# Kernel optimization log

Hardware: AMD Instinct MI355X
Metric: run time of the kernel (lower is better)

## Reference

```python
import jax, jax.numpy as jnp
import numpy as np

B, L, H2, P, A, T = 2048, 128, 600, 50, 50, 3  # batch, seq, 2*hidden, pos_emb, attn, latent types


def setup_inputs() -> dict:
    key = jax.random.key(0)
    ks = jax.random.split(key, 9)
    return {
        "hidden": jax.random.normal(ks[0], (B, L, H2), dtype=jnp.float32),
        "pos1_emb": jax.random.normal(ks[1], (B, L, P), dtype=jnp.float32),
        "pos2_emb": jax.random.normal(ks[2], (B, L, P), dtype=jnp.float32),
        "entity1_idx": jax.random.randint(ks[3], (B,), 0, L),
        "entity2_idx": jax.random.randint(ks[4], (B,), 0, L),
        "W_hid": jax.random.normal(ks[5], (A, H2 + 2 * P), dtype=jnp.float32) * 0.05,
        "W_ent": jax.random.normal(ks[6], (A, 4 * H2), dtype=jnp.float32) * 0.05,
        "latent_types": jax.random.normal(ks[7], (T, H2), dtype=jnp.float32) * 0.05,
        "v": jax.random.normal(ks[8], (A, 1), dtype=jnp.float32) * 0.05,
    }


def _latent_type(ent, latent_types):
    # ent: [B, 1, H2]; latent_types: [T, H2]
    a = jax.nn.softmax(jnp.einsum("bed,td->bet", ent, latent_types), axis=-1)
    return jnp.einsum("bet,td->bed", a, latent_types)  # [B, 1, H2]


def reference(hidden, pos1_emb, pos2_emb, entity1_idx, entity2_idx, W_hid, W_ent, latent_types, v):
    b = hidden.shape[0]
    batch_ix = jnp.arange(b)
    hid_e1 = hidden[batch_ix, entity1_idx][:, None, :]  # [B, 1, H2]
    hid_e2 = hidden[batch_ix, entity2_idx][:, None, :]
    e1_type = _latent_type(hid_e1, latent_types)
    e2_type = _latent_type(hid_e2, latent_types)
    # u1: per-token projection, u2: per-sentence entity projection (broadcast over L)
    u1 = jnp.einsum("bld,ad->bla", jnp.concatenate([hidden, pos1_emb, pos2_emb], axis=-1), W_hid)
    u2 = jnp.einsum("bed,ad->bea", jnp.concatenate([hid_e1, e1_type, hid_e2, e2_type], axis=-1), W_ent)
    u = jnp.tanh(u1 + u2)  # [B, L, A]
    scores = jnp.einsum("bla,a->bl", u, v[:, 0])  # [B, L]
    alpha = jax.nn.softmax(scores, axis=-1)
    z = jnp.einsum("bl,bld->bd", alpha, hidden)  # [B, H2]
    return z
```

## Files before the change

kernel.cpp:

```cpp
#include <hip/hip_runtime.h>
#include <hip/hip_bf16.h>
#include <math.h>


#define B_    2048
#define L_    128
#define H2_   600
#define P_    50
#define A_    50
#define D700  700
#define KCN   22
#define KH    11
#define AP    64
#define MT    16
#define XP    712

typedef __attribute__((ext_vector_type(8))) short short8;
typedef __attribute__((ext_vector_type(4))) float f32x4;

__device__ __forceinline__ unsigned short f2bf(float f) {
  unsigned u = __float_as_uint(f);
  u += 0x7fffu + ((u >> 16) & 1u);
  return (unsigned short)(u >> 16);
}
__device__ __forceinline__ unsigned pk2(float lo, float hi) {
  return (unsigned)f2bf(lo) | ((unsigned)f2bf(hi) << 16);
}
__device__ __forceinline__ float bf2f(unsigned short s) {
  return __uint_as_float(((unsigned)s) << 16);
}

__global__ __launch_bounds__(256) void kwprep(const float* __restrict__ Wh,
                                              unsigned short* __restrict__ Wt) {
  int idx = blockIdx.x * 256 + threadIdx.x;
  if (idx >= KCN * 2048) return;
  int kc = idx >> 11, r = idx & 2047, a = r >> 5, kk = r & 31;
  int d = kc * 32 + kk;
  float v = (a < A_ && d < D700) ? Wh[a * D700 + d] : 0.f;
  Wt[idx] = f2bf(v);
}

__global__ __launch_bounds__(256) void ku2(const float* __restrict__ hidden,
                                           const int* __restrict__ e1,
                                           const int* __restrict__ e2,
                                           const float* __restrict__ Went,
                                           const float* __restrict__ lt,
                                           float* __restrict__ u2ws) {
  __shared__ __align__(16) float E[2][2400];
  __shared__ float dots[2][2][3];
  __shared__ float aw[2][2][3];
  int tid = threadIdx.x;
  int b0 = blockIdx.x * 2;

  for (int idx = tid; idx < 2 * 2 * 150; idx += 256) {
    int i = idx / 300, r = idx - i * 300, e = r / 150, g = r - e * 150;
    int bb = b0 + i;
    int l = e ? e2[bb] : e1[bb];
    float4 f = *(const float4*)(hidden + ((size_t)bb * L_ + l) * H2_ + g * 4);
    *(float4*)(&E[i][e * 1200 + g * 4]) = f;
  }
  __syncthreads();

  int w = tid >> 6, lane = tid & 63;
  for (int task = w * 3; task < w * 3 + 3; ++task) {
    int i = task / 6, e = (task / 3) & 1, t = task % 3;
    float p = 0.f;
    for (int d = lane; d < 600; d += 64) p += E[i][e * 1200 + d] * lt[t * 600 + d];
    #pragma unroll
    for (int mask = 1; mask <= 32; mask <<= 1) p += __shfl_xor(p, mask);
    if (lane == 0) dots[i][e][t] = p;
  }
  __syncthreads();
  if (tid < 12) {
    int t = tid % 3, e = (tid / 3) & 1, i = tid / 6;
    float d0 = dots[i][e][0], d1 = dots[i][e][1], d2 = dots[i][e][2];
    float m = fmaxf(d0, fmaxf(d1, d2));
    float x0 = expf(d0 - m), x1 = expf(d1 - m), x2 = expf(d2 - m);
    float Z = x0 + x1 + x2;
    aw[i][e][t] = ((t == 0) ? x0 : (t == 1) ? x1 : x2) / Z;
  }
  __syncthreads();
  for (int idx = tid; idx < 2 * 2 * 600; idx += 256) {
    int i = idx / 1200, r = idx - i * 1200, e = r / 600, d = r - e * 600;
    float v = aw[i][e][0] * lt[d] + aw[i][e][1] * lt[600 + d] + aw[i][e][2] * lt[1200 + d];
    E[i][e * 1200 + 600 + d] = v;
  }
  __syncthreads();
  for (int a = w; a < A_; a += 4) {
    float acc[2] = {0.f, 0.f};
    for (int d0 = lane * 4; d0 < 2400; d0 += 256) {
      float4 wv = *(const float4*)(Went + a * 2400 + d0);
      #pragma unroll
      for (int i = 0; i < 2; ++i) {
        float4 ev = *(const float4*)(&E[i][d0]);
        acc[i] += ev.x * wv.x + ev.y * wv.y + ev.z * wv.z + ev.w * wv.w;
      }
    }
    #pragma unroll
    for (int i = 0; i < 2; ++i) {
      float p = acc[i];
      #pragma unroll
      for (int mask = 1; mask <= 32; mask <<= 1) p += __shfl_xor(p, mask);
      if (lane == 0) u2ws[(b0 + i) * AP + a] = p;
    }
  }
  for (int idx = tid; idx < 2 * (AP - A_); idx += 256) {
    u2ws[(b0 + idx / (AP - A_)) * AP + A_ + idx % (AP - A_)] = 0.f;
  }
}

__global__ __launch_bounds__(256, 4) void kmain(
    const float* __restrict__ hidden, const float* __restrict__ pos1,
    const float* __restrict__ pos2, const float* __restrict__ vvec,
    const unsigned short* __restrict__ Wt, const float* __restrict__ u2ws,
    float* __restrict__ zp_ws, float* __restrict__ mS_ws) {
  __shared__ __align__(16) unsigned short Xs[MT * XP];
  __shared__ float scores4[4][MT];
  __shared__ float es_s[MT];
  __shared__ float u2s[AP];
  __shared__ float vs[AP];

  int tid = threadIdx.x;
  int bq = blockIdx.x;
  int b = bq >> 3, o = bq & 7, tok0 = o * MT;
  int lane = tid & 63, wv = tid >> 6;
  int acol = lane & 15, kgrp = lane >> 4;

  int t = tid >> 4, c0 = tid & 15;
  const float* rowp = hidden + ((size_t)(b * L_ + tok0) + t) * H2_;
  float4 f[9];
  #pragma unroll
  for (int j = 0; j < 9; ++j) f[j] = *(const float4*)(rowp + (c0 + 16 * j) * 4);
  bool h10 = (c0 < 6);
  float4 f9;
  if (h10) f9 = *(const float4*)(rowp + (c0 + 144) * 4);

  const float* p1 = pos1 + (size_t)(b * L_ + tok0) * P_;
  const float* p2 = pos2 + (size_t)(b * L_ + tok0) * P_;
  float2 q1a = *(const float2*)(p1 + tid * 2);
  float2 q2a = *(const float2*)(p2 + tid * 2);
  bool hq = (tid < 144);
  float2 q1b, q2b;
  if (hq) {
    q1b = *(const float2*)(p1 + (tid + 256) * 2);
    q2b = *(const float2*)(p2 + (tid + 256) * 2);
  }
  float u2v = 0.f, vvv = 0.f;
  if (tid < AP) {
    u2v = u2ws[b * AP + tid];
    vvv = (tid < A_) ? vvec[tid] : 0.f;
  }
  const unsigned short* wbase = Wt + (wv * 16 + acol) * 32 + kgrp * 8;
  short8 wf1[KH];
  #pragma unroll
  for (int kc = 0; kc < KH; ++kc)
    wf1[kc] = *(const short8*)(wbase + kc * 2048);

  #pragma unroll
  for (int j = 0; j < 9; ++j) {
    uint2 w; w.x = pk2(f[j].x, f[j].y); w.y = pk2(f[j].z, f[j].w);
    *(uint2*)(&Xs[t * XP + (c0 + 16 * j) * 4]) = w;
  }
  if (h10) {
    uint2 w; w.x = pk2(f9.x, f9.y); w.y = pk2(f9.z, f9.w);
    *(uint2*)(&Xs[t * XP + (c0 + 144) * 4]) = w;
  }
  {
    int t1 = tid / 25, g = tid - t1 * 25;
    *(unsigned*)(&Xs[t1 * XP + 600 + g * 2]) = pk2(q1a.x, q1a.y);
    *(unsigned*)(&Xs[t1 * XP + 650 + g * 2]) = pk2(q2a.x, q2a.y);
  }
  if (hq) {
    int idx = tid + 256;
    int t1 = idx / 25, g = idx - t1 * 25;
    *(unsigned*)(&Xs[t1 * XP + 600 + g * 2]) = pk2(q1b.x, q1b.y);
    *(unsigned*)(&Xs[t1 * XP + 650 + g * 2]) = pk2(q2b.x, q2b.y);
  }
  if (tid < MT * 2) {
    int tt = tid >> 1, g = tid & 1;
    *(unsigned*)(&Xs[tt * XP + 700 + g * 2]) = 0u;
  }
  if (tid < AP) { u2s[tid] = u2v; vs[tid] = vvv; }
  __syncthreads();

  short8 wf2[KH];
  #pragma unroll
  for (int kc = 0; kc < KH; ++kc)
    wf2[kc] = *(const short8*)(wbase + (KH + kc) * 2048);

  f32x4 acc0 = {0.f, 0.f, 0.f, 0.f};
  #pragma unroll
  for (int kc = 0; kc < KH; ++kc) {
    short8 a0 = *(const short8*)(&Xs[acol * XP + kc * 32 + kgrp * 8]);
    acc0 = __builtin_amdgcn_mfma_f32_16x16x32_bf16(a0, wf1[kc], acc0, 0, 0, 0);
  }
  #pragma unroll
  for (int kc = 0; kc < KH; ++kc) {
    short8 a0 = *(const short8*)(&Xs[acol * XP + (KH + kc) * 32 + kgrp * 8]);
    acc0 = __builtin_amdgcn_mfma_f32_16x16x32_bf16(a0, wf2[kc], acc0, 0, 0, 0);
  }

  {
    float va = vs[wv * 16 + acol];
    float u2a = u2s[wv * 16 + acol];
    float s0[4];
    #pragma unroll
    for (int r = 0; r < 4; ++r) s0[r] = va * tanhf(acc0[r] + u2a);
    #pragma unroll
    for (int mask = 1; mask < 16; mask <<= 1) {
      #pragma unroll
      for (int r = 0; r < 4; ++r) s0[r] += __shfl_xor(s0[r], mask);
    }
    if (acol == 0) {
      #pragma unroll
      for (int r = 0; r < 4; ++r) scores4[wv][kgrp * 4 + r] = s0[r];
    }
  }
  __syncthreads();

  if (tid < 64) {
    float s = (tid < MT)
                  ? (scores4[0][tid] + scores4[1][tid] + scores4[2][tid] + scores4[3][tid])
                  : -3.402823466e38f;
    float m = s;
    #pragma unroll
    for (int mask = 1; mask <= 32; mask <<= 1) m = fmaxf(m, __shfl_xor(m, mask));
    float e = (tid < MT) ? expf(s - m) : 0.f;
    float S = e;
    #pragma unroll
    for (int mask = 1; mask <= 32; mask <<= 1) S += __shfl_xor(S, mask);
    if (tid < MT) es_s[tid] = e;
    if (tid == 0) { mS_ws[bq * 2] = m; mS_ws[bq * 2 + 1] = S; }
  }
  __syncthreads();

  if (tid < 75) {
    float acc[8] = {0.f, 0.f, 0.f, 0.f, 0.f, 0.f, 0.f, 0.f};
    #pragma unroll
    for (int tt = 0; tt < MT; ++tt) {
      short8 xv = *(const short8*)(&Xs[tt * XP + tid * 8]);
      float e = es_s[tt];
      #pragma unroll
      for (int j = 0; j < 8; ++j) acc[j] += e * bf2f((unsigned short)xv[j]);
    }
    float4 w0 = {acc[0], acc[1], acc[2], acc[3]};
    float4 w1 = {acc[4], acc[5], acc[6], acc[7]};
    *(float4*)(zp_ws + (size_t)bq * 600 + tid * 8) = w0;
    *(float4*)(zp_ws + (size_t)bq * 600 + tid * 8 + 4) = w1;
  }
}

__global__ __launch_bounds__(128) void kcomb(const float* __restrict__ zp_ws,
                                             const float* __restrict__ mS_ws,
                                             float* __restrict__ out) {
  int b = blockIdx.x, tid = threadIdx.x;
  float mq[8], Sq[8];
  #pragma unroll
  for (int qq = 0; qq < 8; ++qq) {
    mq[qq] = mS_ws[(b * 8 + qq) * 2];
    Sq[qq] = mS_ws[(b * 8 + qq) * 2 + 1];
  }
  float M = mq[0];
  #pragma unroll
  for (int qq = 1; qq < 8; ++qq) M = fmaxf(M, mq[qq]);
  float c[8], Z = 0.f;
  #pragma unroll
  for (int qq = 0; qq < 8; ++qq) { c[qq] = expf(mq[qq] - M); Z += Sq[qq] * c[qq]; }
  float inv = 1.f / Z;
  for (int d = tid; d < 600; d += 128) {
    float z = 0.f;
    #pragma unroll
    for (int qq = 0; qq < 8; ++qq) z += c[qq] * zp_ws[(size_t)(b * 8 + qq) * 600 + d];
    out[b * 600 + d] = z * inv;
  }
}

extern "C" void kernel_launch(void* const* d_in, const int* in_sizes, int n_in,
                              void* d_out, int out_size, void* d_ws, size_t ws_size,
                              hipStream_t stream) {
  const float* hidden = (const float*)d_in[0];
  const float* pos1   = (const float*)d_in[1];
  const float* pos2   = (const float*)d_in[2];
  const int*   e1     = (const int*)d_in[3];
  const int*   e2     = (const int*)d_in[4];
  const float* Whid   = (const float*)d_in[5];
  const float* Went   = (const float*)d_in[6];
  const float* lt     = (const float*)d_in[7];
  const float* vvec   = (const float*)d_in[8];
  float* out = (float*)d_out;

  char* ws = (char*)d_ws;
  unsigned short* Wt = (unsigned short*)ws;
  float* u2ws  = (float*)(ws + 98304);
  float* mS_ws = (float*)(ws + 98304 + 524288);
  float* zp_ws = (float*)(ws + 98304 + 524288 + 131072);

  hipLaunchKernelGGL(kwprep, dim3(176), dim3(256), 0, stream, Whid, Wt);
  hipLaunchKernelGGL(ku2, dim3(B_ / 2), dim3(256), 0, stream, hidden, e1, e2, Went, lt, u2ws);
  hipLaunchKernelGGL(kmain, dim3(B_ * 8), dim3(256), 0, stream, hidden, pos1, pos2, vvec,
                     Wt, u2ws, zp_ws, mS_ws);
  hipLaunchKernelGGL(kcomb, dim3(B_), dim3(128), 0, stream, zp_ws, mS_ws, out);
}
```

Measured before the change: 272.5 us.

## Make kmain persistent with double-buffered LDS prefetch of next tile

Converts kmain into a persistent kernel with a fixed grid of 768 blocks that loops over token tiles. Each block loads the W fragments into registers once, then prefetches the next tile's hidden and pos rows into a second LDS buffer while it computes the current tile's MFMA, tanh, softmax and weighted sum. The goal is to hide global memory latency and avoid reloading weights for every tile. The cost is twice the LDS, more registers (launch bounds lowered to 3 blocks per SM), and fewer resident blocks, which could reduce memory-level parallelism.

```diff
diff --git a/kernel.cpp b/kernel.cpp
--- a/kernel.cpp
+++ b/kernel.cpp
@@ -10,10 +10,11 @@
 #define A_    50
 #define D700  700
 #define KCN   22
-#define KH    11
 #define AP    64
 #define MT    16
 #define XP    712
+#define GRIDM 768
+#define NBQ   (B_ * 8)
 
 typedef __attribute__((ext_vector_type(8))) short short8;
 typedef __attribute__((ext_vector_type(4))) float f32x4;
@@ -109,144 +110,195 @@
   }
 }
 
-__global__ __launch_bounds__(256, 4) void kmain(
+__global__ __launch_bounds__(256, 3) void kmain(
     const float* __restrict__ hidden, const float* __restrict__ pos1,
     const float* __restrict__ pos2, const float* __restrict__ vvec,
     const unsigned short* __restrict__ Wt, const float* __restrict__ u2ws,
     float* __restrict__ zp_ws, float* __restrict__ mS_ws) {
-  __shared__ __align__(16) unsigned short Xs[MT * XP];
+  __shared__ __align__(16) unsigned short Xs[2][MT * XP];
   __shared__ float scores4[4][MT];
   __shared__ float es_s[MT];
-  __shared__ float u2s[AP];
-  __shared__ float vs[AP];
 
   int tid = threadIdx.x;
+  int lane = tid & 63, wvix = tid >> 6;
+  int acol = lane & 15, kgrp = lane >> 4;
+  int t = tid >> 4, c0 = tid & 15;
+  bool h10 = (c0 < 6);
+  bool hq = (tid < 144);
+  int aidx = wvix * 16 + acol;
+
+  const unsigned short* wbase = Wt + aidx * 32 + kgrp * 8;
+  short8 wf[KCN];
+  #pragma unroll
+  for (int kc = 0; kc < KCN; ++kc) wf[kc] = *(const short8*)(wbase + kc * 2048);
+  float va = (aidx < A_) ? vvec[aidx] : 0.f;
+
+  if (tid < 64) {
+    int hh = tid >> 5, r = tid & 31, rr = r >> 1, g = r & 1;
+    *(unsigned*)(&Xs[hh][rr * XP + 700 + g * 2]) = 0u;
+  }
+
   int bq = blockIdx.x;
-  int b = bq >> 3, o = bq & 7, tok0 = o * MT;
-  int lane = tid & 63, wv = tid >> 6;
-  int acol = lane & 15, kgrp = lane >> 4;
-
-  int t = tid >> 4, c0 = tid & 15;
-  const float* rowp = hidden + ((size_t)(b * L_ + tok0) + t) * H2_;
-  float4 f[9];
-  #pragma unroll
-  for (int j = 0; j < 9; ++j) f[j] = *(const float4*)(rowp + (c0 + 16 * j) * 4);
-  bool h10 = (c0 < 6);
-  float4 f9;
-  if (h10) f9 = *(const float4*)(rowp + (c0 + 144) * 4);
-
-  const float* p1 = pos1 + (size_t)(b * L_ + tok0) * P_;
-  const float* p2 = pos2 + (size_t)(b * L_ + tok0) * P_;
-  float2 q1a = *(const float2*)(p1 + tid * 2);
-  float2 q2a = *(const float2*)(p2 + tid * 2);
-  bool hq = (tid < 144);
-  float2 q1b, q2b;
-  if (hq) {
-    q1b = *(const float2*)(p1 + (tid + 256) * 2);
-    q2b = *(const float2*)(p2 + (tid + 256) * 2);
-  }
-  float u2v = 0.f, vvv = 0.f;
-  if (tid < AP) {
-    u2v = u2ws[b * AP + tid];
-    vvv = (tid < A_) ? vvec[tid] : 0.f;
-  }
-  const unsigned short* wbase = Wt + (wv * 16 + acol) * 32 + kgrp * 8;
-  short8 wf1[KH];
-  #pragma unroll
-  for (int kc = 0; kc < KH; ++kc)
-    wf1[kc] = *(const short8*)(wbase + kc * 2048);
-
-  #pragma unroll
-  for (int j = 0; j < 9; ++j) {
-    uint2 w; w.x = pk2(f[j].x, f[j].y); w.y = pk2(f[j].z, f[j].w);
-    *(uint2*)(&Xs[t * XP + (c0 + 16 * j) * 4]) = w;
-  }
-  if (h10) {
-    uint2 w; w.x = pk2(f9.x, f9.y); w.y = pk2(f9.z, f9.w);
-    *(uint2*)(&Xs[t * XP + (c0 + 144) * 4]) = w;
-  }
+  float u2cur;
   {
-    int t1 = tid / 25, g = tid - t1 * 25;
-    *(unsigned*)(&Xs[t1 * XP + 600 + g * 2]) = pk2(q1a.x, q1a.y);
-    *(unsigned*)(&Xs[t1 * XP + 650 + g * 2]) = pk2(q2a.x, q2a.y);
-  }
-  if (hq) {
-    int idx = tid + 256;
-    int t1 = idx / 25, g = idx - t1 * 25;
-    *(unsigned*)(&Xs[t1 * XP + 600 + g * 2]) = pk2(q1b.x, q1b.y);
-    *(unsigned*)(&Xs[t1 * XP + 650 + g * 2]) = pk2(q2b.x, q2b.y);
-  }
-  if (tid < MT * 2) {
-    int tt = tid >> 1, g = tid & 1;
-    *(unsigned*)(&Xs[tt * XP + 700 + g * 2]) = 0u;
-  }
-  if (tid < AP) { u2s[tid] = u2v; vs[tid] = vvv; }
-  __syncthreads();
-
-  short8 wf2[KH];
-  #pragma unroll
-  for (int kc = 0; kc < KH; ++kc)
-    wf2[kc] = *(const short8*)(wbase + (KH + kc) * 2048);
-
-  f32x4 acc0 = {0.f, 0.f, 0.f, 0.f};
-  #pragma unroll
-  for (int kc = 0; kc < KH; ++kc) {
-    short8 a0 = *(const short8*)(&Xs[acol * XP + kc * 32 + kgrp * 8]);
-    acc0 = __builtin_amdgcn_mfma_f32_16x16x32_bf16(a0, wf1[kc], acc0, 0, 0, 0);
-  }
-  #pragma unroll
-  for (int kc = 0; kc < KH; ++kc) {
-    short8 a0 = *(const short8*)(&Xs[acol * XP + (KH + kc) * 32 + kgrp * 8]);
-    acc0 = __builtin_amdgcn_mfma_f32_16x16x32_bf16(a0, wf2[kc], acc0, 0, 0, 0);
-  }
-
-  {
-    float va = vs[wv * 16 + acol];
-    float u2a = u2s[wv * 16 + acol];
-    float s0[4];
-    #pragma unroll
-    for (int r = 0; r < 4; ++r) s0[r] = va * tanhf(acc0[r] + u2a);
-    #pragma unroll
-    for (int mask = 1; mask < 16; mask <<= 1) {
-      #pragma unroll
-      for (int r = 0; r < 4; ++r) s0[r] += __shfl_xor(s0[r], mask);
-    }
-    if (acol == 0) {
-      #pragma unroll
-      for (int r = 0; r < 4; ++r) scores4[wv][kgrp * 4 + r] = s0[r];
-    }
-  }
-  __syncthreads();
-
-  if (tid < 64) {
-    float s = (tid < MT)
-                  ? (scores4[0][tid] + scores4[1][tid] + scores4[2][tid] + scores4[3][tid])
-                  : -3.402823466e38f;
-    float m = s;
-    #pragma unroll
-    for (int mask = 1; mask <= 32; mask <<= 1) m = fmaxf(m, __shfl_xor(m, mask));
-    float e = (tid < MT) ? expf(s - m) : 0.f;
-    float S = e;
-    #pragma unroll
-    for (int mask = 1; mask <= 32; mask <<= 1) S += __shfl_xor(S, mask);
-    if (tid < MT) es_s[tid] = e;
-    if (tid == 0) { mS_ws[bq * 2] = m; mS_ws[bq * 2 + 1] = S; }
-  }
-  __syncthreads();
-
-  if (tid < 75) {
-    float acc[8] = {0.f, 0.f, 0.f, 0.f, 0.f, 0.f, 0.f, 0.f};
-    #pragma unroll
-    for (int tt = 0; tt < MT; ++tt) {
-      short8 xv = *(const short8*)(&Xs[tt * XP + tid * 8]);
-      float e = es_s[tt];
-      #pragma unroll
-      for (int j = 0; j < 8; ++j) acc[j] += e * bf2f((unsigned short)xv[j]);
-    }
-    float4 w0 = {acc[0], acc[1], acc[2], acc[3]};
-    float4 w1 = {acc[4], acc[5], acc[6], acc[7]};
-    *(float4*)(zp_ws + (size_t)bq * 600 + tid * 8) = w0;
-    *(float4*)(zp_ws + (size_t)bq * 600 + tid * 8 + 4) = w1;
+    int b = bq >> 3, tok0 = (bq & 7) * MT;
+    const float* rowp = hidden + ((size_t)(b * L_ + tok0) + t) * H2_;
+    float4 f[9]; float4 f9 = {0.f, 0.f, 0.f, 0.f};
+    #pragma unroll
+    for (int j = 0; j < 9; ++j) f[j] = *(const float4*)(rowp + (c0 + 16 * j) * 4);
+    if (h10) f9 = *(const float4*)(rowp + (c0 + 144) * 4);
+    const float* p1 = pos1 + (size_t)(b * L_ + tok0) * P_;
+    const float* p2 = pos2 + (size_t)(b * L_ + tok0) * P_;
+    float2 q1a = *(const float2*)(p1 + tid * 2);
+    float2 q2a = *(const float2*)(p2 + tid * 2);
+    float2 q1b = {0.f, 0.f}, q2b = {0.f, 0.f};
+    if (hq) {
+      q1b = *(const float2*)(p1 + (tid + 256) * 2);
+      q2b = *(const float2*)(p2 + (tid + 256) * 2);
+    }
+    u2cur = u2ws[b * AP + aidx];
+    #pragma unroll
+    for (int j = 0; j < 9; ++j) {
+      uint2 w; w.x = pk2(f[j].x, f[j].y); w.y = pk2(f[j].z, f[j].w);
+      *(uint2*)(&Xs[0][t * XP + (c0 + 16 * j) * 4]) = w;
+    }
+    if (h10) {
+      uint2 w; w.x = pk2(f9.x, f9.y); w.y = pk2(f9.z, f9.w);
+      *(uint2*)(&Xs[0][t * XP + (c0 + 144) * 4]) = w;
+    }
+    {
+      int t1 = tid / 25, g = tid - t1 * 25;
+      *(unsigned*)(&Xs[0][t1 * XP + 600 + g * 2]) = pk2(q1a.x, q1a.y);
+      *(unsigned*)(&Xs[0][t1 * XP + 650 + g * 2]) = pk2(q2a.x, q2a.y);
+    }
+    if (hq) {
+      int idx = tid + 256;
+      int t1 = idx / 25, g = idx - t1 * 25;
+      *(unsigned*)(&Xs[0][t1 * XP + 600 + g * 2]) = pk2(q1b.x, q1b.y);
+      *(unsigned*)(&Xs[0][t1 * XP + 650 + g * 2]) = pk2(q2b.x, q2b.y);
+    }
+  }
+  __syncthreads();
+
+  int h = 0;
+  while (true) {
+    int bqn = bq + GRIDM;
+    bool hasnext = (bqn < NBQ);
+    int bn = bqn >> 3, tok0n = (bqn & 7) * MT;
+    const float* rowpn = hidden + ((size_t)(bn * L_ + tok0n) + t) * H2_;
+
+    f32x4 acc = {0.f, 0.f, 0.f, 0.f};
+    #pragma unroll
+    for (int kc = 0; kc < KCN; ++kc) {
+      short8 a0 = *(const short8*)(&Xs[h][acol * XP + kc * 32 + kgrp * 8]);
+      acc = __builtin_amdgcn_mfma_f32_16x16x32_bf16(a0, wf[kc], acc, 0, 0, 0);
+    }
+
+    float4 fA[5];
+    if (hasnext) {
+      #pragma unroll
+      for (int j = 0; j < 5; ++j) fA[j] = *(const float4*)(rowpn + (c0 + 16 * j) * 4);
+    }
+
+    {
+      float s0[4];
+      #pragma unroll
+      for (int r = 0; r < 4; ++r) s0[r] = va * tanhf(acc[r] + u2cur);
+      #pragma unroll
+      for (int mask = 1; mask < 16; mask <<= 1) {
+        #pragma unroll
+        for (int r = 0; r < 4; ++r) s0[r] += __shfl_xor(s0[r], mask);
+      }
+      if (acol == 0) {
+        #pragma unroll
+        for (int r = 0; r < 4; ++r) scores4[wvix][kgrp * 4 + r] = s0[r];
+      }
+    }
+    __syncthreads();
+
+    if (tid < 64) {
+      float s = (tid < MT)
+                    ? (scores4[0][tid] + scores4[1][tid] + scores4[2][tid] + scores4[3][tid])
+                    : -3.402823466e38f;
+      float m = s;
+      #pragma unroll
+      for (int mask = 1; mask <= 32; mask <<= 1) m = fmaxf(m, __shfl_xor(m, mask));
+      float e = (tid < MT) ? expf(s - m) : 0.f;
+      float S = e;
+      #pragma unroll
+      for (int mask = 1; mask <= 32; mask <<= 1) S += __shfl_xor(S, mask);
+      if (tid < MT) es_s[tid] = e;
+      if (tid == 0) { mS_ws[bq * 2] = m; mS_ws[bq * 2 + 1] = S; }
+    }
+
+    float4 fB[5] = {};
+    float2 q1a = {0.f, 0.f}, q2a = {0.f, 0.f}, q1b = {0.f, 0.f}, q2b = {0.f, 0.f};
+    float u2n = 0.f;
+    if (hasnext) {
+      #pragma unroll
+      for (int j = 0; j < 4; ++j) fB[j] = *(const float4*)(rowpn + (c0 + 16 * (5 + j)) * 4);
+      if (h10) fB[4] = *(const float4*)(rowpn + (c0 + 144) * 4);
+      const float* p1n = pos1 + (size_t)(bn * L_ + tok0n) * P_;
+      const float* p2n = pos2 + (size_t)(bn * L_ + tok0n) * P_;
+      q1a = *(const float2*)(p1n + tid * 2);
+      q2a = *(const float2*)(p2n + tid * 2);
+      if (hq) {
+        q1b = *(const float2*)(p1n + (tid + 256) * 2);
+        q2b = *(const float2*)(p2n + (tid + 256) * 2);
+      }
+      u2n = u2ws[bn * AP + aidx];
+      unsigned short* Xn = &Xs[h ^ 1][0];
+      #pragma unroll
+      for (int j = 0; j < 5; ++j) {
+        uint2 w; w.x = pk2(fA[j].x, fA[j].y); w.y = pk2(fA[j].z, fA[j].w);
+        *(uint2*)(&Xn[t * XP + (c0 + 16 * j) * 4]) = w;
+      }
+    }
+    __syncthreads();
+
+    if (tid < 75) {
+      float zacc[8] = {0.f, 0.f, 0.f, 0.f, 0.f, 0.f, 0.f, 0.f};
+      #pragma unroll
+      for (int tt = 0; tt < MT; ++tt) {
+        short8 xv = *(const short8*)(&Xs[h][tt * XP + tid * 8]);
+        float e = es_s[tt];
+        #pragma unroll
+        for (int j = 0; j < 8; ++j) zacc[j] += e * bf2f((unsigned short)xv[j]);
+      }
+      float4 w0 = {zacc[0], zacc[1], zacc[2], zacc[3]};
+      float4 w1 = {zacc[4], zacc[5], zacc[6], zacc[7]};
+      *(float4*)(zp_ws + (size_t)bq * 600 + tid * 8) = w0;
+      *(float4*)(zp_ws + (size_t)bq * 600 + tid * 8 + 4) = w1;
+    }
+
+    if (hasnext) {
+      unsigned short* Xn = &Xs[h ^ 1][0];
+      #pragma unroll
+      for (int j = 0; j < 4; ++j) {
+        uint2 w; w.x = pk2(fB[j].x, fB[j].y); w.y = pk2(fB[j].z, fB[j].w);
+        *(uint2*)(&Xn[t * XP + (c0 + 16 * (5 + j)) * 4]) = w;
+      }
+      if (h10) {
+        uint2 w; w.x = pk2(fB[4].x, fB[4].y); w.y = pk2(fB[4].z, fB[4].w);
+        *(uint2*)(&Xn[t * XP + (c0 + 144) * 4]) = w;
+      }
+      {
+        int t1 = tid / 25, g = tid - t1 * 25;
+        *(unsigned*)(&Xn[t1 * XP + 600 + g * 2]) = pk2(q1a.x, q1a.y);
+        *(unsigned*)(&Xn[t1 * XP + 650 + g * 2]) = pk2(q2a.x, q2a.y);
+      }
+      if (hq) {
+        int idx = tid + 256;
+        int t1 = idx / 25, g = idx - t1 * 25;
+        *(unsigned*)(&Xn[t1 * XP + 600 + g * 2]) = pk2(q1b.x, q1b.y);
+        *(unsigned*)(&Xn[t1 * XP + 650 + g * 2]) = pk2(q2b.x, q2b.y);
+      }
+      u2cur = u2n;
+    }
+    __syncthreads();
+    if (!hasnext) break;
+    h ^= 1;
+    bq = bqn;
   }
 }
 
@@ -297,7 +349,7 @@
 
   hipLaunchKernelGGL(kwprep, dim3(176), dim3(256), 0, stream, Whid, Wt);
   hipLaunchKernelGGL(ku2, dim3(B_ / 2), dim3(256), 0, stream, hidden, e1, e2, Went, lt, u2ws);
-  hipLaunchKernelGGL(kmain, dim3(B_ * 8), dim3(256), 0, stream, hidden, pos1, pos2, vvec,
+  hipLaunchKernelGGL(kmain, dim3(GRIDM), dim3(256), 0, stream, hidden, pos1, pos2, vvec,
                      Wt, u2ws, zp_ws, mS_ws);
   hipLaunchKernelGGL(kcomb, dim3(B_), dim3(128), 0, stream, zp_ws, mS_ws, out);
 }
```

Result: slower. 419.5 us (+53.9%).
